# Optimization experiments

Hardware: AMD Instinct MI355X
Metric: run time of the kernel (lower is better)

The kernel has to match this reference:

```python
import jax, jax.numpy as jnp
import numpy as np

HIDDEN = 1024

def setup_inputs() -> dict:
    key = jax.random.key(0)
    ks = jax.random.split(key, 7)
    scale = 1.0 / np.sqrt(HIDDEN)
    x = jax.random.normal(ks[0], (4, 2048, HIDDEN), dtype=jnp.float32)
    Wq = jax.random.uniform(ks[1], (HIDDEN, HIDDEN), jnp.float32, -scale, scale)
    bq = jax.random.uniform(ks[2], (HIDDEN,), jnp.float32, -scale, scale)
    Wk = jax.random.uniform(ks[3], (HIDDEN, HIDDEN), jnp.float32, -scale, scale)
    bk = jax.random.uniform(ks[4], (HIDDEN,), jnp.float32, -scale, scale)
    Wv = jax.random.uniform(ks[5], (HIDDEN, HIDDEN), jnp.float32, -scale, scale)
    bv = jax.random.uniform(ks[6], (HIDDEN,), jnp.float32, -scale, scale)
    return {"x": x, "Wq": Wq, "bq": bq, "Wk": Wk, "bk": bk, "Wv": Wv, "bv": bv}

def reference(x, Wq, bq, Wk, bk, Wv, bv):
    # x: [n, t, e]; weights stored as [in, out] so y = x @ W + b
    q = jnp.einsum('nte,ef->ntf', x, Wq) + bq
    k = jnp.einsum('nte,ef->ntf', x, Wk) + bk
    v = jnp.einsum('nte,ef->ntf', x, Wv) + bv
    scores = jnp.einsum('nqe,nke->nqk', q, k)  # unscaled, as in the original
    alpha = jax.nn.softmax(scores, axis=2)
    return jnp.einsum('nqk,nke->nqe', alpha, v)
```

## Files before the change

kernel.cpp:

```cpp
#include <hip/hip_runtime.h>
#include <stdint.h>

typedef __attribute__((ext_vector_type(4))) float f32x4;
typedef __attribute__((ext_vector_type(8))) _Float16 f16x8;

#define HIDDEN 1024
#define SEQ 2048
#define NB 4

__device__ inline unsigned short f2h_bits(float f) {
    _Float16 h = (_Float16)f;
    return __builtin_bit_cast(unsigned short, h);
}

__device__ inline void gload16(const void* g, void* l) {
    __builtin_amdgcn_global_load_lds(
        (const __attribute__((address_space(1))) unsigned int*)g,
        (__attribute__((address_space(3))) unsigned int*)l,
        16, 0, 0);
}

template<int N> __device__ inline void waitvm() {
    if constexpr (N == 0) asm volatile("s_waitcnt vmcnt(0)" ::: "memory");
    else if constexpr (N == 2) asm volatile("s_waitcnt vmcnt(2)" ::: "memory");
    else if constexpr (N == 3) asm volatile("s_waitcnt vmcnt(3)" ::: "memory");
    else if constexpr (N == 4) asm volatile("s_waitcnt vmcnt(4)" ::: "memory");
    else if constexpr (N == 6) asm volatile("s_waitcnt vmcnt(6)" ::: "memory");
    else static_assert(N == 0, "bad vmcnt");
}
__device__ inline void waitlgkm0() { asm volatile("s_waitcnt lgkmcnt(0)" ::: "memory"); }

template<int BM, int BN, int BIAS_MODE, bool OUT_F16, int MINW>
__global__ __launch_bounds__(512, MINW) void gemm8p(
    const unsigned short* __restrict__ A, int lda,
    const unsigned short* __restrict__ Bt, int ldb,
    const float* __restrict__ bias,
    void* __restrict__ Cptr, int ldc, int K,
    long long aBatch, long long bBatch, long long cBatch)
{
    constexpr int MR = BM / 32;
    constexpr int NRW = BN / 64;
    constexpr int LA = BM / 128;
    constexpr int LB = BN / 128;
    constexpr int LP = LA + LB;
    constexpr int ASLICE = BM * 32;
    constexpr int BSLICE = BN * 32;
    constexpr int BOFF = 4 * ASLICE;

    extern __shared__ unsigned short lds[];

    const int tid = threadIdx.x, lane = tid & 63, wave = tid >> 6;
    const int wr = wave >> 2, wc = wave & 3;
    const int fr = lane & 15, fq = lane >> 4;

    const int gx = gridDim.x, gy = gridDim.y;
    const int nwg = gx * gy * gridDim.z;
    const int id = (blockIdx.z * gy + blockIdx.y) * gx + blockIdx.x;
    const int id2 = (id & 7) * (nwg >> 3) + (id >> 3);
    const int bx = id2 % gx;
    const int by = (id2 / gx) % gy;
    const long long bz = id2 / (gx * gy);

    const unsigned short* Ab = A + bz * aBatch + (long long)(by * BM) * lda;
    const unsigned short* Bb = Bt + bz * bBatch + (long long)(bx * BN) * ldb;

    const unsigned short* sA[LA]; int dA[LA];
    #pragma unroll
    for (int i = 0; i < LA; ++i) {
        int c = i * 512 + tid; int r = c >> 2; int ls = (c & 3) ^ ((r >> 1) & 3);
        sA[i] = Ab + (long long)r * lda + ls * 8;
        dA[i] = (i * 512 + wave * 64) * 16;
    }
    const unsigned short* sB[LB]; int dB[LB];
    #pragma unroll
    for (int i = 0; i < LB; ++i) {
        int c = i * 512 + tid; int r = c >> 2; int ls = (c & 3) ^ ((r >> 1) & 3);
        sB[i] = Bb + (long long)r * ldb + ls * 8;
        dB[i] = (i * 512 + wave * 64) * 16;
    }

    auto stage = [&](int t, int ks) {
        int buf = t & 1;
        int aoff = ((buf * 2 + ks) * ASLICE) * 2;
        int boff = (BOFF + (buf * 2 + ks) * BSLICE) * 2;
        int kof = t * 64 + ks * 32;
        #pragma unroll
        for (int i = 0; i < LA; ++i) gload16(sA[i] + kof, (char*)lds + aoff + dA[i]);
        #pragma unroll
        for (int i = 0; i < LB; ++i) gload16(sB[i] + kof, (char*)lds + boff + dB[i]);
    };

    const int NT = K / 64;
    stage(0, 0); stage(0, 1); stage(1, 0);

    f32x4 acc[MR][NRW] = {};

    for (int t = 0; t < NT; ++t) {
        #pragma unroll
        for (int ks = 0; ks < 2; ++ks) {
            if (t == NT - 1) { if (ks == 0) waitvm<LP>(); else waitvm<0>(); }
            else waitvm<2 * LP>();
            __builtin_amdgcn_s_barrier();
            __builtin_amdgcn_sched_barrier(0);

            const int buf = t & 1;
            const unsigned short* as = lds + (buf * 2 + ks) * ASLICE;
            const unsigned short* bs = lds + BOFF + (buf * 2 + ks) * BSLICE;
            f16x8 af[MR], bf[NRW];
            #pragma unroll
            for (int m = 0; m < MR; ++m) {
                int r = wr * (BM / 2) + m * 16 + fr;
                int es = fq ^ ((r >> 1) & 3);
                af[m] = *(const f16x8*)&as[r * 32 + es * 8];
            }
            #pragma unroll
            for (int n = 0; n < NRW; ++n) {
                int r = wc * (BN / 4) + n * 16 + fr;
                int es = fq ^ ((r >> 1) & 3);
                bf[n] = *(const f16x8*)&bs[r * 32 + es * 8];
            }
            if (ks == 0) { if (t + 1 < NT) stage(t + 1, 1); }
            else         { if (t + 2 < NT) stage(t + 2, 0); }

            waitlgkm0();
            __builtin_amdgcn_sched_barrier(0);
            __builtin_amdgcn_s_setprio(1);
            #pragma unroll
            for (int m = 0; m < MR; ++m)
                #pragma unroll
                for (int n = 0; n < NRW; ++n)
                    acc[m][n] = __builtin_amdgcn_mfma_f32_16x16x32_f16(af[m], bf[n], acc[m][n], 0, 0, 0);
            __builtin_amdgcn_s_setprio(0);
        }
    }

    const int row0 = by * BM + wr * (BM / 2);
    const int col0 = bx * BN + wc * (BN / 4);
    #pragma unroll
    for (int m = 0; m < MR; ++m)
        #pragma unroll
        for (int n = 0; n < NRW; ++n)
            #pragma unroll
            for (int i = 0; i < 4; ++i) {
                int r = row0 + m * 16 + fq * 4 + i;
                int c = col0 + n * 16 + fr;
                float v = acc[m][n][i];
                if constexpr (BIAS_MODE == 1) v += bias[c];
                if constexpr (BIAS_MODE == 2) v += bias[r];
                if constexpr (OUT_F16)
                    ((unsigned short*)Cptr + bz * cBatch)[(long long)r * ldc + c] = f2h_bits(v);
                else
                    ((float*)Cptr + bz * cBatch)[(long long)r * ldc + c] = v;
            }
}

__global__ __launch_bounds__(256) void cvt_f32_f16(const float* __restrict__ in,
                                                   unsigned short* __restrict__ out, int n8)
{
    int i = blockIdx.x * blockDim.x + threadIdx.x;
    if (i >= n8) return;
    const float4* p = (const float4*)in + (long long)i * 2;
    float4 a = p[0], b = p[1];
    ushort4 o0, o1;
    o0.x = f2h_bits(a.x); o0.y = f2h_bits(a.y); o0.z = f2h_bits(a.z); o0.w = f2h_bits(a.w);
    o1.x = f2h_bits(b.x); o1.y = f2h_bits(b.y); o1.z = f2h_bits(b.z); o1.w = f2h_bits(b.w);
    ushort4* o = (ushort4*)out + (long long)i * 2;
    o[0] = o0; o[1] = o1;
}

__global__ void transpose_cvt(const float* __restrict__ in, unsigned short* __restrict__ out,
                              int R, int C)
{
    __shared__ unsigned short t[32][33];
    const int bx = blockIdx.x * 32;
    const int by = blockIdx.y * 32;
    const int xT = threadIdx.x, yT = threadIdx.y;
    #pragma unroll
    for (int i = 0; i < 32; i += 8)
        t[yT + i][xT] = f2h_bits(in[(long long)(by + yT + i) * C + bx + xT]);
    __syncthreads();
    #pragma unroll
    for (int i = 0; i < 32; i += 8)
        out[(long long)(bx + yT + i) * R + by + xT] = t[xT][yT + i];
}

__global__ void concat_bias2(const float* __restrict__ bq, const float* __restrict__ bk,
                             float* __restrict__ cb)
{
    int i = threadIdx.x;
    cb[i] = bq[i];
    cb[HIDDEN + i] = bk[i];
}

__global__ __launch_bounds__(256) void softmax_inplace(float* __restrict__ S)
{
    const int tid = threadIdx.x;
    float* row = S + (long long)blockIdx.x * SEQ;
    float4 a = ((const float4*)row)[tid];
    float4 b = ((const float4*)row)[tid + 256];
    float vv[8] = {a.x, a.y, a.z, a.w, b.x, b.y, b.z, b.w};

    float mx = vv[0];
    #pragma unroll
    for (int j = 1; j < 8; ++j) mx = fmaxf(mx, vv[j]);
    #pragma unroll
    for (int o = 32; o > 0; o >>= 1) mx = fmaxf(mx, __shfl_xor(mx, o));
    __shared__ float redm[4], reds[4];
    if ((tid & 63) == 0) redm[tid >> 6] = mx;
    __syncthreads();
    mx = fmaxf(fmaxf(redm[0], redm[1]), fmaxf(redm[2], redm[3]));

    float ev[8], sum = 0.f;
    #pragma unroll
    for (int j = 0; j < 8; ++j) { ev[j] = __expf(vv[j] - mx); sum += ev[j]; }
    #pragma unroll
    for (int o = 32; o > 0; o >>= 1) sum += __shfl_xor(sum, o);
    if ((tid & 63) == 0) reds[tid >> 6] = sum;
    __syncthreads();
    sum = reds[0] + reds[1] + reds[2] + reds[3];
    float inv = 1.0f / sum;

    unsigned short* rb = (unsigned short*)row;
    ushort4 o0, o1;
    o0.x = f2h_bits(ev[0] * inv); o0.y = f2h_bits(ev[1] * inv);
    o0.z = f2h_bits(ev[2] * inv); o0.w = f2h_bits(ev[3] * inv);
    o1.x = f2h_bits(ev[4] * inv); o1.y = f2h_bits(ev[5] * inv);
    o1.z = f2h_bits(ev[6] * inv); o1.w = f2h_bits(ev[7] * inv);
    *(ushort4*)&rb[(long long)tid * 4] = o0;
    *(ushort4*)&rb[((long long)tid + 256) * 4] = o1;
}

extern "C" void kernel_launch(void* const* d_in, const int* in_sizes, int n_in,
                              void* d_out, int out_size, void* d_ws, size_t ws_size,
                              hipStream_t stream)
{
    (void)in_sizes; (void)n_in; (void)out_size; (void)ws_size;
    const float* x  = (const float*)d_in[0];
    const float* Wq = (const float*)d_in[1];
    const float* bq = (const float*)d_in[2];
    const float* Wk = (const float*)d_in[3];
    const float* bk = (const float*)d_in[4];
    const float* Wv = (const float*)d_in[5];
    const float* bv = (const float*)d_in[6];
    float* out = (float*)d_out;

    (void)hipFuncSetAttribute(reinterpret_cast<const void*>(&gemm8p<128, 256, 1, true, 2>),
                              hipFuncAttributeMaxDynamicSharedMemorySize, 98304);
    (void)hipFuncSetAttribute(reinterpret_cast<const void*>(&gemm8p<128, 256, 2, true, 2>),
                              hipFuncAttributeMaxDynamicSharedMemorySize, 98304);
    (void)hipFuncSetAttribute(reinterpret_cast<const void*>(&gemm8p<128, 256, 0, false, 2>),
                              hipFuncAttributeMaxDynamicSharedMemorySize, 98304);
    (void)hipFuncSetAttribute(reinterpret_cast<const void*>(&gemm8p<128, 128, 0, false, 4>),
                              hipFuncAttributeMaxDynamicSharedMemorySize, 65536);

    char* ws = (char*)d_ws;
    const long long MTOT = (long long)NB * SEQ;

    unsigned short* qk = (unsigned short*)ws;
    unsigned short* vt = (unsigned short*)(ws + (size_t)MTOT * 2048 * 2);
    char* sreg = ws + (size_t)MTOT * 2048 * 2 + (size_t)HIDDEN * MTOT * 2;
    unsigned short* wt = (unsigned short*)sreg;
    float* cb = (float*)(sreg + (size_t)3 * HIDDEN * HIDDEN * 2);
    unsigned short* xh = (unsigned short*)(sreg + (size_t)3 * HIDDEN * HIDDEN * 2 + 8192);
    float* S = (float*)sreg;

    {
        int n8 = (int)(MTOT * HIDDEN / 8);
        cvt_f32_f16<<<dim3((n8 + 255) / 256), 256, 0, stream>>>(x, xh, n8);
    }
    dim3 tb(32, 8), tg(HIDDEN / 32, HIDDEN / 32);
    transpose_cvt<<<tg, tb, 0, stream>>>(Wq, wt,                       HIDDEN, HIDDEN);
    transpose_cvt<<<tg, tb, 0, stream>>>(Wk, wt +     HIDDEN * HIDDEN, HIDDEN, HIDDEN);
    transpose_cvt<<<tg, tb, 0, stream>>>(Wv, wt + 2 * HIDDEN * HIDDEN, HIDDEN, HIDDEN);
    concat_bias2<<<1, 1024, 0, stream>>>(bq, bk, cb);

    gemm8p<128, 256, 1, true, 2><<<dim3(2048 / 256, (unsigned)(MTOT / 128), 1), 512, 98304, stream>>>(
        xh, HIDDEN, wt, HIDDEN, cb, qk, 2048, HIDDEN, 0, 0, 0);

    gemm8p<128, 256, 2, true, 2><<<dim3((unsigned)(MTOT / 256), HIDDEN / 128, 1), 512, 98304, stream>>>(
        wt + 2 * HIDDEN * HIDDEN, HIDDEN, xh, HIDDEN, bv, vt, (int)MTOT, HIDDEN, 0, 0, 0);

    for (int b0 = 0; b0 < NB; b0 += 2) {
        const unsigned short* q  = qk + (long long)b0 * SEQ * 2048;
        const unsigned short* km = q + HIDDEN;
        gemm8p<128, 256, 0, false, 2><<<dim3(SEQ / 256, SEQ / 128, 2), 512, 98304, stream>>>(
            q, 2048, km, 2048, nullptr, S, SEQ, HIDDEN,
            (long long)SEQ * 2048, (long long)SEQ * 2048, (long long)SEQ * SEQ);
        softmax_inplace<<<dim3(2 * SEQ), 256, 0, stream>>>(S);
        const unsigned short* P = (const unsigned short*)S;
        const unsigned short* Bv = vt + (long long)b0 * SEQ;
        float* Ob = out + (long long)b0 * SEQ * HIDDEN;
        gemm8p<128, 128, 0, false, 4><<<dim3(HIDDEN / 128, SEQ / 128, 2), 512, 65536, stream>>>(
            P, 2 * SEQ, Bv, (int)MTOT, nullptr, Ob, HIDDEN, SEQ,
            (long long)SEQ * 2 * SEQ, (long long)SEQ, (long long)SEQ * HIDDEN);
    }
}
```

Before: 206.6 us.

## Restructure GEMM pipeline into 4-slot ring with split MFMA halves and wave templating

Replaces the double-buffered two-substep K loop with a four-slot ring of 32-wide K slices, keeping three loads in flight. Each step loads the A fragments in two halves with a barrier between the MFMA halves, so LDS reads overlap with matrix work. Wave layout is now a template parameter: the QK projection uses 256x256 tiles, and the PV GEMM drops to 256 threads (2x2 waves). The aim is better load/compute overlap and fewer redundant loads, at the cost of more LDS, an extra barrier per step, and register pressure in the larger tile.

```diff
diff --git a/kernel.cpp b/kernel.cpp
--- a/kernel.cpp
+++ b/kernel.cpp
@@ -22,26 +22,28 @@
 
 template<int N> __device__ inline void waitvm() {
     if constexpr (N == 0) asm volatile("s_waitcnt vmcnt(0)" ::: "memory");
-    else if constexpr (N == 2) asm volatile("s_waitcnt vmcnt(2)" ::: "memory");
     else if constexpr (N == 3) asm volatile("s_waitcnt vmcnt(3)" ::: "memory");
     else if constexpr (N == 4) asm volatile("s_waitcnt vmcnt(4)" ::: "memory");
     else if constexpr (N == 6) asm volatile("s_waitcnt vmcnt(6)" ::: "memory");
+    else if constexpr (N == 8) asm volatile("s_waitcnt vmcnt(8)" ::: "memory");
     else static_assert(N == 0, "bad vmcnt");
 }
 __device__ inline void waitlgkm0() { asm volatile("s_waitcnt lgkmcnt(0)" ::: "memory"); }
 
-template<int BM, int BN, int BIAS_MODE, bool OUT_F16, int MINW>
-__global__ __launch_bounds__(512, MINW) void gemm8p(
+template<int BM, int BN, int WM, int WN, int BIAS_MODE, bool OUT_F16, int MINW>
+__global__ __launch_bounds__(WM * WN * 64, MINW) void gemm8p(
     const unsigned short* __restrict__ A, int lda,
     const unsigned short* __restrict__ Bt, int ldb,
     const float* __restrict__ bias,
     void* __restrict__ Cptr, int ldc, int K,
     long long aBatch, long long bBatch, long long cBatch)
 {
-    constexpr int MR = BM / 32;
-    constexpr int NRW = BN / 64;
-    constexpr int LA = BM / 128;
-    constexpr int LB = BN / 128;
+    constexpr int THREADS = WM * WN * 64;
+    constexpr int MR = BM / (WM * 16);
+    constexpr int NRW = BN / (WN * 16);
+    constexpr int MH = MR / 2;
+    constexpr int LA = 4 * BM / THREADS;
+    constexpr int LB = 4 * BN / THREADS;
     constexpr int LP = LA + LB;
     constexpr int ASLICE = BM * 32;
     constexpr int BSLICE = BN * 32;
@@ -50,7 +52,7 @@
     extern __shared__ unsigned short lds[];
 
     const int tid = threadIdx.x, lane = tid & 63, wave = tid >> 6;
-    const int wr = wave >> 2, wc = wave & 3;
+    const int wr = wave / WN, wc = wave % WN;
     const int fr = lane & 15, fq = lane >> 4;
 
     const int gx = gridDim.x, gy = gridDim.y;
@@ -67,75 +69,89 @@
     const unsigned short* sA[LA]; int dA[LA];
     #pragma unroll
     for (int i = 0; i < LA; ++i) {
-        int c = i * 512 + tid; int r = c >> 2; int ls = (c & 3) ^ ((r >> 1) & 3);
+        int c = i * THREADS + tid; int r = c >> 2; int ls = (c & 3) ^ ((r >> 1) & 3);
         sA[i] = Ab + (long long)r * lda + ls * 8;
-        dA[i] = (i * 512 + wave * 64) * 16;
+        dA[i] = (i * THREADS + wave * 64) * 16;
     }
     const unsigned short* sB[LB]; int dB[LB];
     #pragma unroll
     for (int i = 0; i < LB; ++i) {
-        int c = i * 512 + tid; int r = c >> 2; int ls = (c & 3) ^ ((r >> 1) & 3);
+        int c = i * THREADS + tid; int r = c >> 2; int ls = (c & 3) ^ ((r >> 1) & 3);
         sB[i] = Bb + (long long)r * ldb + ls * 8;
-        dB[i] = (i * 512 + wave * 64) * 16;
-    }
-
-    auto stage = [&](int t, int ks) {
-        int buf = t & 1;
-        int aoff = ((buf * 2 + ks) * ASLICE) * 2;
-        int boff = (BOFF + (buf * 2 + ks) * BSLICE) * 2;
-        int kof = t * 64 + ks * 32;
-        #pragma unroll
-        for (int i = 0; i < LA; ++i) gload16(sA[i] + kof, (char*)lds + aoff + dA[i]);
-        #pragma unroll
-        for (int i = 0; i < LB; ++i) gload16(sB[i] + kof, (char*)lds + boff + dB[i]);
+        dB[i] = (i * THREADS + wave * 64) * 16;
+    }
+
+    auto stage = [&](int q) {
+        int slot = q & 3;
+        int kof = q * 32;
+        #pragma unroll
+        for (int i = 0; i < LA; ++i)
+            gload16(sA[i] + kof, (char*)lds + slot * (ASLICE * 2) + dA[i]);
+        #pragma unroll
+        for (int i = 0; i < LB; ++i)
+            gload16(sB[i] + kof, (char*)lds + (BOFF + slot * BSLICE) * 2 + dB[i]);
     };
 
-    const int NT = K / 64;
-    stage(0, 0); stage(0, 1); stage(1, 0);
+    const int NPAIR = K / 32;
+    stage(0); stage(1); stage(2);
 
     f32x4 acc[MR][NRW] = {};
 
-    for (int t = 0; t < NT; ++t) {
-        #pragma unroll
-        for (int ks = 0; ks < 2; ++ks) {
-            if (t == NT - 1) { if (ks == 0) waitvm<LP>(); else waitvm<0>(); }
-            else waitvm<2 * LP>();
-            __builtin_amdgcn_s_barrier();
-            __builtin_amdgcn_sched_barrier(0);
-
-            const int buf = t & 1;
-            const unsigned short* as = lds + (buf * 2 + ks) * ASLICE;
-            const unsigned short* bs = lds + BOFF + (buf * 2 + ks) * BSLICE;
-            f16x8 af[MR], bf[NRW];
+    for (int p = 0; p < NPAIR; ++p) {
+        if (p == NPAIR - 1) waitvm<0>();
+        else if (p == NPAIR - 2) waitvm<LP>();
+        else waitvm<2 * LP>();
+        __builtin_amdgcn_s_barrier();
+        __builtin_amdgcn_sched_barrier(0);
+
+        const int slot = p & 3;
+        const unsigned short* as = lds + slot * ASLICE;
+        const unsigned short* bs = lds + BOFF + slot * BSLICE;
+
+        f16x8 af[MR], bf[NRW];
+        #pragma unroll
+        for (int n = 0; n < NRW; ++n) {
+            int r = wc * (BN / WN) + n * 16 + fr;
+            int es = fq ^ ((r >> 1) & 3);
+            bf[n] = *(const f16x8*)&bs[r * 32 + es * 8];
+        }
+        #pragma unroll
+        for (int m = 0; m < MH; ++m) {
+            int r = wr * (BM / WM) + m * 16 + fr;
+            int es = fq ^ ((r >> 1) & 3);
+            af[m] = *(const f16x8*)&as[r * 32 + es * 8];
+        }
+        if (p + 3 < NPAIR) stage(p + 3);
+        waitlgkm0();
+        __builtin_amdgcn_sched_barrier(0);
+        __builtin_amdgcn_s_setprio(1);
+        #pragma unroll
+        for (int m = 0; m < MH; ++m)
             #pragma unroll
-            for (int m = 0; m < MR; ++m) {
-                int r = wr * (BM / 2) + m * 16 + fr;
-                int es = fq ^ ((r >> 1) & 3);
-                af[m] = *(const f16x8*)&as[r * 32 + es * 8];
-            }
+            for (int n = 0; n < NRW; ++n)
+                acc[m][n] = __builtin_amdgcn_mfma_f32_16x16x32_f16(af[m], bf[n], acc[m][n], 0, 0, 0);
+        __builtin_amdgcn_s_setprio(0);
+
+        #pragma unroll
+        for (int m = MH; m < MR; ++m) {
+            int r = wr * (BM / WM) + m * 16 + fr;
+            int es = fq ^ ((r >> 1) & 3);
+            af[m] = *(const f16x8*)&as[r * 32 + es * 8];
+        }
+        __builtin_amdgcn_s_barrier();
+        waitlgkm0();
+        __builtin_amdgcn_sched_barrier(0);
+        __builtin_amdgcn_s_setprio(1);
+        #pragma unroll
+        for (int m = MH; m < MR; ++m)
             #pragma unroll
-            for (int n = 0; n < NRW; ++n) {
-                int r = wc * (BN / 4) + n * 16 + fr;
-                int es = fq ^ ((r >> 1) & 3);
-                bf[n] = *(const f16x8*)&bs[r * 32 + es * 8];
-            }
-            if (ks == 0) { if (t + 1 < NT) stage(t + 1, 1); }
-            else         { if (t + 2 < NT) stage(t + 2, 0); }
-
-            waitlgkm0();
-            __builtin_amdgcn_sched_barrier(0);
-            __builtin_amdgcn_s_setprio(1);
-            #pragma unroll
-            for (int m = 0; m < MR; ++m)
-                #pragma unroll
-                for (int n = 0; n < NRW; ++n)
-                    acc[m][n] = __builtin_amdgcn_mfma_f32_16x16x32_f16(af[m], bf[n], acc[m][n], 0, 0, 0);
-            __builtin_amdgcn_s_setprio(0);
-        }
-    }
-
-    const int row0 = by * BM + wr * (BM / 2);
-    const int col0 = bx * BN + wc * (BN / 4);
+            for (int n = 0; n < NRW; ++n)
+                acc[m][n] = __builtin_amdgcn_mfma_f32_16x16x32_f16(af[m], bf[n], acc[m][n], 0, 0, 0);
+        __builtin_amdgcn_s_setprio(0);
+    }
+
+    const int row0 = by * BM + wr * (BM / WM);
+    const int col0 = bx * BN + wc * (BN / WN);
     #pragma unroll
     for (int m = 0; m < MR; ++m)
         #pragma unroll
@@ -244,13 +260,13 @@
     const float* bv = (const float*)d_in[6];
     float* out = (float*)d_out;
 
-    (void)hipFuncSetAttribute(reinterpret_cast<const void*>(&gemm8p<128, 256, 1, true, 2>),
+    (void)hipFuncSetAttribute(reinterpret_cast<const void*>(&gemm8p<256, 256, 2, 4, 1, true, 2>),
+                              hipFuncAttributeMaxDynamicSharedMemorySize, 131072);
+    (void)hipFuncSetAttribute(reinterpret_cast<const void*>(&gemm8p<128, 256, 2, 4, 2, true, 2>),
                               hipFuncAttributeMaxDynamicSharedMemorySize, 98304);
-    (void)hipFuncSetAttribute(reinterpret_cast<const void*>(&gemm8p<128, 256, 2, true, 2>),
+    (void)hipFuncSetAttribute(reinterpret_cast<const void*>(&gemm8p<128, 256, 2, 4, 0, false, 2>),
                               hipFuncAttributeMaxDynamicSharedMemorySize, 98304);
-    (void)hipFuncSetAttribute(reinterpret_cast<const void*>(&gemm8p<128, 256, 0, false, 2>),
-                              hipFuncAttributeMaxDynamicSharedMemorySize, 98304);
-    (void)hipFuncSetAttribute(reinterpret_cast<const void*>(&gemm8p<128, 128, 0, false, 4>),
+    (void)hipFuncSetAttribute(reinterpret_cast<const void*>(&gemm8p<128, 128, 2, 2, 0, false, 2>),
                               hipFuncAttributeMaxDynamicSharedMemorySize, 65536);
 
     char* ws = (char*)d_ws;
@@ -274,23 +290,23 @@
     transpose_cvt<<<tg, tb, 0, stream>>>(Wv, wt + 2 * HIDDEN * HIDDEN, HIDDEN, HIDDEN);
     concat_bias2<<<1, 1024, 0, stream>>>(bq, bk, cb);
 
-    gemm8p<128, 256, 1, true, 2><<<dim3(2048 / 256, (unsigned)(MTOT / 128), 1), 512, 98304, stream>>>(
+    gemm8p<256, 256, 2, 4, 1, true, 2><<<dim3(2048 / 256, (unsigned)(MTOT / 256), 1), 512, 131072, stream>>>(
         xh, HIDDEN, wt, HIDDEN, cb, qk, 2048, HIDDEN, 0, 0, 0);
 
-    gemm8p<128, 256, 2, true, 2><<<dim3((unsigned)(MTOT / 256), HIDDEN / 128, 1), 512, 98304, stream>>>(
+    gemm8p<128, 256, 2, 4, 2, true, 2><<<dim3((unsigned)(MTOT / 256), HIDDEN / 128, 1), 512, 98304, stream>>>(
         wt + 2 * HIDDEN * HIDDEN, HIDDEN, xh, HIDDEN, bv, vt, (int)MTOT, HIDDEN, 0, 0, 0);
 
     for (int b0 = 0; b0 < NB; b0 += 2) {
         const unsigned short* q  = qk + (long long)b0 * SEQ * 2048;
         const unsigned short* km = q + HIDDEN;
-        gemm8p<128, 256, 0, false, 2><<<dim3(SEQ / 256, SEQ / 128, 2), 512, 98304, stream>>>(
+        gemm8p<128, 256, 2, 4, 0, false, 2><<<dim3(SEQ / 256, SEQ / 128, 2), 512, 98304, stream>>>(
             q, 2048, km, 2048, nullptr, S, SEQ, HIDDEN,
             (long long)SEQ * 2048, (long long)SEQ * 2048, (long long)SEQ * SEQ);
         softmax_inplace<<<dim3(2 * SEQ), 256, 0, stream>>>(S);
         const unsigned short* P = (const unsigned short*)S;
         const unsigned short* Bv = vt + (long long)b0 * SEQ;
         float* Ob = out + (long long)b0 * SEQ * HIDDEN;
-        gemm8p<128, 128, 0, false, 4><<<dim3(HIDDEN / 128, SEQ / 128, 2), 512, 65536, stream>>>(
+        gemm8p<128, 128, 2, 2, 0, false, 2><<<dim3(HIDDEN / 128, SEQ / 128, 2), 256, 65536, stream>>>(
             P, 2 * SEQ, Bv, (int)MTOT, nullptr, Ob, HIDDEN, SEQ,
             (long long)SEQ * 2 * SEQ, (long long)SEQ, (long long)SEQ * HIDDEN);
     }
```

Measured after the change: 202.0 us. -2.2%, faster.
